# Performance work log

Hardware: AMD Instinct MI355X
Metric: run time of the kernel (lower is better)

Reference implementation:

```python
import jax, jax.numpy as jnp
import numpy as np

B, N, E1, H, D = 16, 256, 4, 8, 128  # batch, max nodes, edge types+1, heads, dim
VOCAB = 100


def setup_inputs() -> dict:
    key = jax.random.key(0)
    ks = jax.random.split(key, 20)
    s = 0.05
    return dict(
        node_feat=jax.random.randint(ks[0], (B, N), 0, VOCAB),
        L=jax.random.normal(ks[1], (B, N, N, E1), jnp.float32),
        emb=jax.random.normal(ks[2], (VOCAB, D), jnp.float32) * s,
        W0=jax.random.normal(ks[3], (E1, H, D, D), jnp.float32) * s,
        W1=jax.random.normal(ks[4], (E1, H, D * H * E1, D), jnp.float32) * (s / 4.0),
        a1w0=jax.random.normal(ks[5], (E1, H, D), jnp.float32) * s,
        a1b0=jnp.zeros((E1, H), jnp.float32),
        a2w0=jax.random.normal(ks[6], (E1, H, D), jnp.float32) * s,
        a2b0=jnp.zeros((E1, H), jnp.float32),
        a1w1=jax.random.normal(ks[7], (E1, H, D), jnp.float32) * s,
        a1b1=jnp.zeros((E1, H), jnp.float32),
        a2w1=jax.random.normal(ks[8], (E1, H, D), jnp.float32) * s,
        a2b1=jnp.zeros((E1, H), jnp.float32),
        sb0=jnp.zeros((E1, H, D), jnp.float32),
        sb1=jnp.zeros((E1, H, D), jnp.float32),
        outW=jax.random.normal(ks[9], (D, D), jnp.float32) * s,
        outb=jnp.zeros((D,), jnp.float32),
        attW=jax.random.normal(ks[10], (D,), jnp.float32) * s,
        attb=jnp.zeros((), jnp.float32),
    )


def _gat_layer(state, Ltr, W, a1w, a1b, a2w, a2b, sb, last):
    # state: (B, N, Din); W: (E1, H, Din, D); Ltr: (E1, 1, B, N, N)
    Wh = jnp.einsum('bni,ehio->ehbno', state, W)                      # (E1,H,B,N,D)
    s1 = jnp.einsum('ehbno,eho->ehbn', Wh, a1w) + a1b[:, :, None, None]
    s2 = jnp.einsum('ehbno,eho->ehbn', Wh, a2w) + a2b[:, :, None, None]
    logits = jax.nn.leaky_relu(s1[..., :, None] + s2[..., None, :], 0.2) + Ltr
    att = jax.nn.softmax(logits, axis=3)  # torch softmax over dim=1 of (B,N,N)
    h = jnp.einsum('ehbnm,ehbmo->ehbno', att, Wh) + sb[:, :, None, None, :]
    if last:
        return jnp.mean(h, axis=(0, 1))                               # (B,N,D)
    h = jax.nn.elu(h)
    # concat order in torch: outer edge-type jj, inner head ii -> (B,N,E1*H*D)
    return jnp.transpose(h, (2, 3, 0, 1, 4)).reshape(state.shape[0], state.shape[1], -1)


def reference(node_feat, L, emb, W0, W1, a1w0, a1b0, a2w0, a2b0,
              a1w1, a1b1, a2w1, a2b1, sb0, sb1, outW, outb, attW, attb):
    Ltr = jnp.transpose(L, (3, 0, 1, 2))[:, None]  # (E1,1,B,N,N)
    state = emb[node_feat]                         # (B,N,D)
    state = _gat_layer(state, Ltr, W0, a1w0, a1b0, a2w0, a2b0, sb0, last=False)
    state = _gat_layer(state, Ltr, W1, a1w1, a1b1, a2w1, a2b1, sb1, last=True)
    y = state @ outW + outb                        # (B,N,D)
    aw = jax.nn.sigmoid(state @ attW + attb)       # (B,N)
    y = aw[..., None] * y
    return jnp.mean(y, axis=1)                     # (B,D)
```

## Files before the change

### kernel.cpp

```cpp
#include <hip/hip_runtime.h>
#include <hip/hip_bf16.h>

#define Bq 16
#define Nq 256
#define E1q 4
#define Hq 8
#define Dq 128
#define EH 32
#define BN 4096

typedef __hip_bfloat16 bf16;
typedef short bf16x8 __attribute__((ext_vector_type(8)));
typedef float f32x4 __attribute__((ext_vector_type(4)));

__device__ __forceinline__ void gll16(const void* gptr, void* lptr) {
    __builtin_amdgcn_global_load_lds(
        (const __attribute__((address_space(1))) void*)gptr,
        (__attribute__((address_space(3))) void*)lptr, 16, 0, 0);
}

__device__ __forceinline__ unsigned short f2bf(float v) {
    __hip_bfloat16 h = __float2bfloat16(v);
    return *(unsigned short*)&h;
}

__device__ __forceinline__ void transpose_tile(const float* __restrict__ W,
                                               bf16* __restrict__ WT, int K,
                                               int kt, int nt, int eh,
                                               float (*tile)[65], int tid) {
    int tr = tid >> 6, tc = tid & 63;
    const float* src = W + ((size_t)eh * K + kt * 64) * 128 + nt * 64;
#pragma unroll
    for (int p = 0; p < 16; ++p) {
        int r = p * 4 + tr;
        tile[r][tc] = src[(size_t)r * 128 + tc];
    }
    __syncthreads();
    bf16* dst = WT + ((size_t)eh * 128 + nt * 64) * K + kt * 64;
#pragma unroll
    for (int p = 0; p < 16; ++p) {
        int n = p * 4 + tr;
        dst[(size_t)n * K + tc] = __float2bfloat16(tile[tc][n]);
    }
}

__global__ __launch_bounds__(256) void prep_kernel(const int* __restrict__ nf,
                                                   const float* __restrict__ emb,
                                                   const float* __restrict__ W0,
                                                   const float* __restrict__ W1,
                                                   const float* __restrict__ L,
                                                   bf16* __restrict__ st0b,
                                                   bf16* __restrict__ W0T,
                                                   bf16* __restrict__ W1T,
                                                   float* __restrict__ Le) {
    int bid = blockIdx.x;
    int t = threadIdx.x;
    __shared__ float tile[64][65];
    if (bid < 2048) {
        int i = bid * 256 + t;
        int row = i >> 7, col = i & 127;
        st0b[i] = __float2bfloat16(emb[nf[row] * Dq + col]);
    } else if (bid < 2176) {
        int id2 = bid - 2048;
        transpose_tile(W0, W0T, 128, id2 & 1, (id2 >> 1) & 1, id2 >> 2, tile, t);
    } else if (bid < 6272) {
        int id3 = bid - 2176;
        transpose_tile(W1, W1T, 4096, id3 & 63, (id3 >> 6) & 1, id3 >> 7, tile, t);
    } else {
        int idx = (bid - 6272) * 256 + t;
        float4 v = *(const float4*)(L + (size_t)idx * 4);
        Le[idx] = v.x;
        Le[1048576 + idx] = v.y;
        Le[2097152 + idx] = v.z;
        Le[3145728 + idx] = v.w;
    }
}

__global__ __launch_bounds__(256) void mfma_gemm_kernel(const bf16* __restrict__ Ab,
                                                        const bf16* __restrict__ Bt,
                                                        bf16* __restrict__ Wht,
                                                        const float* __restrict__ a1w,
                                                        const float* __restrict__ a1b,
                                                        const float* __restrict__ a2w,
                                                        const float* __restrict__ a2b,
                                                        float* __restrict__ s1,
                                                        float* __restrict__ s2, int K) {
    int id = blockIdx.x;
    int xcd = id & 7, slot = id >> 3;
    int eh = (slot & 3) * 8 + xcd;
    int rt = slot >> 2;
    int tid = threadIdx.x;
    int w = tid >> 6, l = tid & 63;
    int q = l >> 4, mn = l & 15;
    __shared__ __align__(16) bf16 As[128 * 64];
    __shared__ __align__(16) bf16 Bs[128 * 64];
    __shared__ float red1[128], red2[128];
    const bf16* Ap = Ab + (size_t)(rt * 128) * K;
    const bf16* Bp = Bt + (size_t)eh * 128 * K;
    int lr = l >> 3;
    int g = (l & 7) ^ lr;
    int gcol = g * 8;

    if (tid < 128) { red1[tid] = 0.f; red2[tid] = 0.f; }

    f32x4 acc[4][4];
#pragma unroll
    for (int i = 0; i < 4; i++)
#pragma unroll
        for (int j = 0; j < 4; j++) acc[i][j] = (f32x4){0.f, 0.f, 0.f, 0.f};

    int wr = (w >> 1) * 64, wc = (w & 1) * 64;
    int msw = mn & 7;

    for (int k0 = 0; k0 < K; k0 += 64) {
#pragma unroll
        for (int u = 0; u < 4; ++u) {
            int i = w * 4 + u;
            int r = i * 8 + lr;
            gll16(Ap + (size_t)r * K + k0 + gcol, (char*)As + i * 1024);
            gll16(Bp + (size_t)r * K + k0 + gcol, (char*)Bs + i * 1024);
        }
        __syncthreads();
#pragma unroll
        for (int kk = 0; kk < 2; ++kk) {
            int qb = ((kk * 4 + q) ^ msw) * 16;
            bf16x8 af[4], bfr[4];
#pragma unroll
            for (int i = 0; i < 4; ++i) {
                af[i]  = *(const bf16x8*)((const char*)As + (wr + i * 16 + mn) * 128 + qb);
                bfr[i] = *(const bf16x8*)((const char*)Bs + (wc + i * 16 + mn) * 128 + qb);
            }
#pragma unroll
            for (int i = 0; i < 4; ++i)
#pragma unroll
                for (int j = 0; j < 4; ++j)
                    acc[i][j] = __builtin_amdgcn_mfma_f32_16x16x32_bf16(af[i], bfr[j], acc[i][j], 0, 0, 0);
        }
        __syncthreads();
    }
#pragma unroll
    for (int i = 0; i < 4; ++i) {
        int r0 = rt * 128 + wr + i * 16 + q * 4;
        int b = r0 >> 8, m = r0 & 255;
#pragma unroll
        for (int j = 0; j < 4; ++j) {
            int o = wc + j * 16 + mn;
            ushort4 pk;
            pk.x = f2bf(acc[i][j][0]);
            pk.y = f2bf(acc[i][j][1]);
            pk.z = f2bf(acc[i][j][2]);
            pk.w = f2bf(acc[i][j][3]);
            *(ushort4*)(Wht + ((((size_t)eh * 16 + b) * 128 + o) * 256 + m)) = pk;
        }
    }
    float w1v[4], w2v[4];
#pragma unroll
    for (int j = 0; j < 4; ++j) {
        int o = wc + j * 16 + mn;
        w1v[j] = a1w[eh * 128 + o];
        w2v[j] = a2w[eh * 128 + o];
    }
#pragma unroll
    for (int i = 0; i < 4; ++i)
#pragma unroll
        for (int r = 0; r < 4; ++r) {
            float p1 = 0.f, p2 = 0.f;
#pragma unroll
            for (int j = 0; j < 4; ++j) {
                p1 += acc[i][j][r] * w1v[j];
                p2 += acc[i][j][r] * w2v[j];
            }
#pragma unroll
            for (int off = 1; off < 16; off <<= 1) {
                p1 += __shfl_xor(p1, off);
                p2 += __shfl_xor(p2, off);
            }
            if (mn == 0) {
                int row = wr + i * 16 + q * 4 + r;
                atomicAdd(&red1[row], p1);
                atomicAdd(&red2[row], p2);
            }
        }
    __syncthreads();
    if (tid < 128) {
        int rg = rt * 128 + tid;
        s1[eh * 4096 + rg] = red1[tid] + a1b[eh];
        s2[eh * 4096 + rg] = red2[tid] + a2b[eh];
    }
}

__global__ __launch_bounds__(512, 2) void gemm4k_kernel(const bf16* __restrict__ Ab,
                                                        const bf16* __restrict__ Bt,
                                                        bf16* __restrict__ Wht,
                                                        const float* __restrict__ a1w,
                                                        const float* __restrict__ a1b,
                                                        const float* __restrict__ a2w,
                                                        const float* __restrict__ a2b,
                                                        float* __restrict__ s1,
                                                        float* __restrict__ s2) {
    __shared__ __align__(16) char smem[131072];
    int bid = blockIdx.x;
    int wg = (bid & 7) * 32 + (bid >> 3);
    int tm = wg >> 4, tn = wg & 15;
    int tid = threadIdx.x;
    int wid = tid >> 6, l = tid & 63;
    int wr = wid >> 2, wc = wid & 3;
    int lhi = l >> 4, llo = l & 15;
    int skq = (l & 7) ^ ((l >> 3) & 7);

    const bf16* Ap = Ab + (size_t)tm * 256 * 4096;
    const bf16* Bp = Bt + (size_t)tn * 256 * 4096;
    const bf16* sA = Ap + (size_t)(wid * 8 + (l >> 3)) * 4096 + skq * 8;
    const bf16* sB = Bp + (size_t)(wid * 8 + (l >> 3)) * 4096 + skq * 8;
    char* dA = (char*)smem + wid * 1024;
    char* dB = (char*)smem + 32768 + wid * 1024;

    auto stA = [&](int tt, int s) {
        gll16(sA + (size_t)s * 64 * 4096 + tt * 64, dA + (tt & 1) * 65536 + s * 8192);
    };
    auto stB = [&](int tt, int s) {
        gll16(sB + (size_t)s * 64 * 4096 + tt * 64, dB + (tt & 1) * 65536 + s * 8192);
    };

    f32x4 acc[8][4];
#pragma unroll
    for (int i = 0; i < 8; ++i)
#pragma unroll
        for (int j = 0; j < 4; ++j) acc[i][j] = (f32x4){0.f, 0.f, 0.f, 0.f};

    int kp0 = ((lhi)     ^ (llo & 7)) << 4;
    int kp1 = ((4 + lhi) ^ (llo & 7)) << 4;
    int aoff = (wr * 64 + llo) << 7;
    int boff = 32768 + ((wc * 32 + llo) << 7);

    stA(0, 0); stA(0, 1); stB(0, 0); stB(0, 1);
    stA(0, 2); stA(0, 3); stB(0, 2); stB(0, 3);
    asm volatile("s_waitcnt vmcnt(4)" ::: "memory");
    __builtin_amdgcn_s_barrier();

#pragma unroll 1
    for (int t = 0; t < 64; ++t) {
        const char* sm = (const char*)smem + (t & 1) * 65536;
        bf16x8 A0[4][2], A1[4][2], B0[2][2], B1[2][2];
#pragma unroll
        for (int m = 0; m < 4; ++m) {
            A0[m][0] = *(const bf16x8*)(sm + aoff + m * 2048 + kp0);
            A0[m][1] = *(const bf16x8*)(sm + aoff + m * 2048 + kp1);
        }
#pragma unroll
        for (int n = 0; n < 2; ++n) {
            B0[n][0] = *(const bf16x8*)(sm + boff + n * 2048 + kp0);
            B0[n][1] = *(const bf16x8*)(sm + boff + n * 2048 + kp1);
        }
        if (t < 63) { stA(t + 1, 0); stA(t + 1, 1); }
        asm volatile("s_waitcnt lgkmcnt(8)" ::: "memory");
        __builtin_amdgcn_s_barrier();
        asm volatile("s_waitcnt lgkmcnt(0)" ::: "memory");
        __builtin_amdgcn_sched_barrier(0);
        __builtin_amdgcn_s_setprio(1);
#pragma unroll
        for (int ks = 0; ks < 2; ++ks)
#pragma unroll
            for (int m = 0; m < 4; ++m)
#pragma unroll
                for (int n = 0; n < 2; ++n)
                    acc[m][n] = __builtin_amdgcn_mfma_f32_16x16x32_bf16(A0[m][ks], B0[n][ks], acc[m][n], 0, 0, 0);
        __builtin_amdgcn_s_setprio(0);
        if (t < 63) { asm volatile("s_waitcnt vmcnt(4)" ::: "memory"); }
        else        { asm volatile("s_waitcnt vmcnt(2)" ::: "memory"); }
        __builtin_amdgcn_s_barrier();
#pragma unroll
        for (int m = 0; m < 4; ++m) {
            A1[m][0] = *(const bf16x8*)(sm + aoff + 16384 + m * 2048 + kp0);
            A1[m][1] = *(const bf16x8*)(sm + aoff + 16384 + m * 2048 + kp1);
        }
        if (t < 63) { stB(t + 1, 0); stB(t + 1, 1); }
        __builtin_amdgcn_s_barrier();
        asm volatile("s_waitcnt lgkmcnt(0)" ::: "memory");
        __builtin_amdgcn_sched_barrier(0);
        __builtin_amdgcn_s_setprio(1);
#pragma unroll
        for (int ks = 0; ks < 2; ++ks)
#pragma unroll
            for (int m = 0; m < 4; ++m)
#pragma unroll
                for (int n = 0; n < 2; ++n)
                    acc[4 + m][n] = __builtin_amdgcn_mfma_f32_16x16x32_bf16(A1[m][ks], B0[n][ks], acc[4 + m][n], 0, 0, 0);
        __builtin_amdgcn_s_setprio(0);
        if (t < 63) { asm volatile("s_waitcnt vmcnt(4)" ::: "memory"); }
        else        { asm volatile("s_waitcnt vmcnt(0)" ::: "memory"); }
        __builtin_amdgcn_s_barrier();
#pragma unroll
        for (int n = 0; n < 2; ++n) {
            B1[n][0] = *(const bf16x8*)(sm + boff + 16384 + n * 2048 + kp0);
            B1[n][1] = *(const bf16x8*)(sm + boff + 16384 + n * 2048 + kp1);
        }
        if (t < 63) { stA(t + 1, 2); stA(t + 1, 3); }
        __builtin_amdgcn_s_barrier();
        asm volatile("s_waitcnt lgkmcnt(0)" ::: "memory");
        __builtin_amdgcn_sched_barrier(0);
        __builtin_amdgcn_s_setprio(1);
#pragma unroll
        for (int ks = 0; ks < 2; ++ks)
#pragma unroll
            for (int m = 0; m < 4; ++m)
#pragma unroll
                for (int n = 0; n < 2; ++n)
                    acc[m][2 + n] = __builtin_amdgcn_mfma_f32_16x16x32_bf16(A0[m][ks], B1[n][ks], acc[m][2 + n], 0, 0, 0);
        __builtin_amdgcn_s_setprio(0);
        __builtin_amdgcn_s_barrier();
        if (t < 63) { stB(t + 1, 2); stB(t + 1, 3); }
        __builtin_amdgcn_s_setprio(1);
#pragma unroll
        for (int ks = 0; ks < 2; ++ks)
#pragma unroll
            for (int m = 0; m < 4; ++m)
#pragma unroll
                for (int n = 0; n < 2; ++n)
                    acc[4 + m][2 + n] = __builtin_amdgcn_mfma_f32_16x16x32_bf16(A1[m][ks], B1[n][ks], acc[4 + m][2 + n], 0, 0, 0);
        __builtin_amdgcn_s_setprio(0);
        if (t < 63) { asm volatile("s_waitcnt vmcnt(4)" ::: "memory"); }
        __builtin_amdgcn_s_barrier();
    }

    float* red = (float*)smem;
    red[tid] = 0.f;
    red[tid + 512] = 0.f;
    float w1v[4], w2v[4];
#pragma unroll
    for (int n = 0; n < 4; ++n) {
        int eh = tn * 2 + (n >> 1);
        int o = wc * 32 + (n & 1) * 16 + llo;
        w1v[n] = a1w[eh * 128 + o];
        w2v[n] = a2w[eh * 128 + o];
    }
    __syncthreads();
#pragma unroll
    for (int mi = 0; mi < 8; ++mi) {
        int R = (mi >> 2) * 128 + wr * 64 + (mi & 3) * 16 + lhi * 4;
#pragma unroll
        for (int n = 0; n < 4; ++n) {
            int eh = tn * 2 + (n >> 1);
            int o = wc * 32 + (n & 1) * 16 + llo;
            ushort4 pk;
            pk.x = f2bf(acc[mi][n][0]);
            pk.y = f2bf(acc[mi][n][1]);
            pk.z = f2bf(acc[mi][n][2]);
            pk.w = f2bf(acc[mi][n][3]);
            *(ushort4*)(Wht + ((((size_t)eh * 16 + tm) * 128 + o) * 256 + R)) = pk;
        }
#pragma unroll
        for (int r = 0; r < 4; ++r) {
            float p10 = acc[mi][0][r] * w1v[0] + acc[mi][1][r] * w1v[1];
            float p11 = acc[mi][2][r] * w1v[2] + acc[mi][3][r] * w1v[3];
            float p20 = acc[mi][0][r] * w2v[0] + acc[mi][1][r] * w2v[1];
            float p21 = acc[mi][2][r] * w2v[2] + acc[mi][3][r] * w2v[3];
#pragma unroll
            for (int off = 1; off < 16; off <<= 1) {
                p10 += __shfl_xor(p10, off);
                p11 += __shfl_xor(p11, off);
                p20 += __shfl_xor(p20, off);
                p21 += __shfl_xor(p21, off);
            }
            if (llo == 0) {
                int row = R + r;
                atomicAdd(&red[row], p10);
                atomicAdd(&red[256 + row], p11);
                atomicAdd(&red[512 + row], p20);
                atomicAdd(&red[768 + row], p21);
            }
        }
    }
    __syncthreads();
    {
        int ehl = tid >> 8, row = tid & 255;
        int eh = tn * 2 + ehl;
        s1[eh * 4096 + tm * 256 + row] = red[ehl * 256 + row] + a1b[eh];
        s2[eh * 4096 + tm * 256 + row] = red[512 + ehl * 256 + row] + a2b[eh];
    }
}

__global__ __launch_bounds__(256) void colsoft_kernel(const float* __restrict__ s1,
                                                      const float* __restrict__ s2,
                                                      const float* __restrict__ Le,
                                                      float4* __restrict__ stat) {
    int mt = blockIdx.x, b = blockIdx.y, e = blockIdx.z;
    int t = threadIdx.x;
    __shared__ float Lt[256 * 32];
    __shared__ float s1L[8 * 256];
#pragma unroll
    for (int i = 0; i < 8; ++i) s1L[i * 256 + t] = s1[(e * 8 + i) * 4096 + b * 256 + t];
    const float* Lb = Le + ((size_t)(e * 16 + b) * 256) * 256 + mt * 32;
#pragma unroll
    for (int j = 0; j < 8; ++j) {
        int f = t + 256 * j;
        int n = f >> 3, c4 = (f & 7) * 4;
        *(float4*)(Lt + n * 32 + c4) = *(const float4*)(Lb + (size_t)n * 256 + c4);
    }
    __syncthreads();
    int h = t >> 5, mm = t & 31;
    int m = mt * 32 + mm;
    float s2v = s2[(e * 8 + h) * 4096 + b * 256 + m];
    const float* s1p = s1L + h * 256;
    float s1max = -1e30f;
#pragma unroll
    for (int u = 0; u < 8; ++u) s1max = fmaxf(s1max, s1p[mm * 8 + u]);
#pragma unroll
    for (int off = 16; off; off >>= 1) s1max = fmaxf(s1max, __shfl_xor(s1max, off));
    float sm = s1max + s2v;
    float bound = (sm > 0.f ? sm : 0.2f * sm) + 8.0f;
    float sum = 0.f;
    for (int n = 0; n < 256; ++n) {
        float x = s1p[n] + s2v;
        x = x > 0.f ? x : 0.2f * x;
        x += Lt[n * 32 + mm];
        sum += __expf(x - bound);
    }
    float4 st = {s2v, bound, 1.0f / sum, 0.f};
    stat[(e * 8 + h) * 4096 + b * 256 + m] = st;
}

template <int LAST>
__global__ __launch_bounds__(256) void att_mfma_kernel(const float* __restrict__ s1,
                                                       const float4* __restrict__ stat,
                                                       const float* __restrict__ Le,
                                                       const bf16* __restrict__ Wht,
                                                       const float* __restrict__ sb,
                                                       bf16* __restrict__ outb) {
    int nt = blockIdx.x;
    int b = blockIdx.y;
    int eh = blockIdx.z;
    int e = eh >> 3;
    int tid = threadIdx.x;
    int w = tid >> 6, l = tid & 63;
    int q = l >> 4, mn = l & 15;
    __shared__ __align__(16) bf16 As[128 * 32];
    __shared__ __align__(16) bf16 Bs[128 * 40];
    __shared__ float s1L[128];
    __shared__ __align__(16) float4 stL[256];

    int base = eh * 4096 + b * 256;
    if (tid < 128) s1L[tid] = s1[base + nt * 128 + tid];
    stL[tid] = stat[base + tid];
    __syncthreads();

    const bf16* Whtp = Wht + ((size_t)eh * 16 + b) * 32768;
    int nl = tid >> 1, mh = (tid & 1) * 16;
    const float* Lrow = Le + (((size_t)(e * 16 + b) * 256) + nt * 128 + nl) * 256;
    float s1v = s1L[nl];
    int srow = l >> 2;
    int sq = (l & 3) ^ ((l >> 3) & 3);
    int scol = sq * 8;
    int rsw = ((mn >> 1) & 3) << 3;

    f32x4 acc[4][4];
#pragma unroll
    for (int i = 0; i < 4; i++)
#pragma unroll
        for (int j = 0; j < 4; j++) acc[i][j] = (f32x4){0.f, 0.f, 0.f, 0.f};

    int wr = (w >> 1) * 64, wc = (w & 1) * 64;

    float4 lv[4];
#pragma unroll
    for (int jj = 0; jj < 4; ++jj) lv[jj] = *(const float4*)(Lrow + mh + jj * 4);

    for (int k0 = 0; k0 < 256; k0 += 32) {
#pragma unroll
        for (int u = 0; u < 2; ++u) {
            int i = 2 * w + u;
            gll16(Whtp + (size_t)(i * 16 + srow) * 256 + k0 + scol, (char*)As + i * 1024);
        }
        float4 cur[4];
#pragma unroll
        for (int jj = 0; jj < 4; ++jj) cur[jj] = lv[jj];
        if (k0 + 32 < 256) {
#pragma unroll
            for (int jj = 0; jj < 4; ++jj)
                lv[jj] = *(const float4*)(Lrow + k0 + 32 + mh + jj * 4);
        }
#pragma unroll
        for (int jj = 0; jj < 4; ++jj) {
            int mb = mh + jj * 4;
            float av[4];
#pragma unroll
            for (int c = 0; c < 4; ++c) {
                int m = k0 + mb + c;
                float4 stv = stL[m];
                float x = s1v + stv.x;
                x = x > 0.f ? x : 0.2f * x;
                x += ((const float*)&cur[jj])[c];
                av[c] = __expf(x - stv.y) * stv.z;
            }
            unsigned int u01 = (unsigned int)f2bf(av[0]) | ((unsigned int)f2bf(av[1]) << 16);
            unsigned int u23 = (unsigned int)f2bf(av[2]) | ((unsigned int)f2bf(av[3]) << 16);
            unsigned int* bp = (unsigned int*)Bs + (nl * 40 + mb) / 2;
            bp[0] = u01;
            bp[1] = u23;
        }
        __syncthreads();
        bf16x8 af[4], bfr[4];
#pragma unroll
        for (int i = 0; i < 4; ++i) {
            af[i]  = *(const bf16x8*)(As + (wr + i * 16 + mn) * 32 + ((q << 3) ^ rsw));
            bfr[i] = *(const bf16x8*)(Bs + (wc + i * 16 + mn) * 40 + q * 8);
        }
#pragma unroll
        for (int i = 0; i < 4; ++i)
#pragma unroll
            for (int j = 0; j < 4; ++j)
                acc[i][j] = __builtin_amdgcn_mfma_f32_16x16x32_bf16(af[i], bfr[j], acc[i][j], 0, 0, 0);
        __syncthreads();
    }
#pragma unroll
    for (int i = 0; i < 4; ++i) {
        int o0 = wr + i * 16 + q * 4;
        float4 sbv = *(const float4*)(sb + eh * 128 + o0);
#pragma unroll
        for (int j = 0; j < 4; ++j) {
            int n = wc + j * 16 + mn;
            float v0 = acc[i][j][0] + sbv.x;
            float v1 = acc[i][j][1] + sbv.y;
            float v2 = acc[i][j][2] + sbv.z;
            float v3 = acc[i][j][3] + sbv.w;
            if (LAST == 0) {
                v0 = v0 > 0.f ? v0 : __expf(v0) - 1.f;
                v1 = v1 > 0.f ? v1 : __expf(v1) - 1.f;
                v2 = v2 > 0.f ? v2 : __expf(v2) - 1.f;
                v3 = v3 > 0.f ? v3 : __expf(v3) - 1.f;
                ushort4 pk = {f2bf(v0), f2bf(v1), f2bf(v2), f2bf(v3)};
                *(ushort4*)(outb + (size_t)(b * 256 + nt * 128 + n) * 4096 + eh * Dq + o0) = pk;
            } else {
                ushort4 pk = {f2bf(v0), f2bf(v1), f2bf(v2), f2bf(v3)};
                *(ushort4*)(outb + ((size_t)eh * 4096 + b * 256 + nt * 128 + n) * Dq + o0) = pk;
            }
        }
    }
}

__global__ __launch_bounds__(256) void reduce_aw_kernel(const bf16* __restrict__ h2b,
                                                        const float* __restrict__ attW,
                                                        const float* __restrict__ attb,
                                                        float* __restrict__ st2,
                                                        float* __restrict__ aw) {
    int t = threadIdx.x;
    int rl = t >> 7, o = t & 127;
    int r = blockIdx.x * 2 + rl;
    float acc = 0.f;
#pragma unroll
    for (int eh = 0; eh < EH; ++eh)
        acc += __bfloat162float(h2b[((size_t)eh * 4096 + r) * 128 + o]);
    acc *= (1.0f / 32.0f);
    st2[(size_t)r * 128 + o] = acc;
    float p = acc * attW[o];
#pragma unroll
    for (int off = 32; off; off >>= 1) p += __shfl_down(p, off);
    __shared__ float part[4];
    if ((t & 63) == 0) part[t >> 6] = p;
    __syncthreads();
    if (t == 0) aw[r] = 1.0f / (1.0f + __expf(-(part[0] + part[1] + attb[0])));
    if (t == 128) aw[r] = 1.0f / (1.0f + __expf(-(part[2] + part[3] + attb[0])));
}

__global__ __launch_bounds__(128) void final_kernel(const float* __restrict__ st2,
                                                    const float* __restrict__ aw,
                                                    const float* __restrict__ outW,
                                                    const float* __restrict__ outb,
                                                    float* __restrict__ out) {
    int b = blockIdx.x;
    int t = threadIdx.x;
    __shared__ float awL[256], zL[128];
    awL[t] = aw[b * 256 + t];
    awL[t + 128] = aw[b * 256 + t + 128];
    __syncthreads();
    float z = 0.f;
    for (int n = 0; n < 256; ++n) z += awL[n] * st2[(size_t)(b * 256 + n) * Dq + t];
    float sa = 0.f;
    for (int n = 0; n < 256; ++n) sa += awL[n];
    zL[t] = z;
    __syncthreads();
    float acc = sa * outb[t];
    for (int o = 0; o < Dq; ++o) acc += zL[o] * outW[o * Dq + t];
    out[b * Dq + t] = acc * (1.0f / 256.0f);
}

extern "C" void kernel_launch(void* const* d_in, const int* in_sizes, int n_in,
                              void* d_out, int out_size, void* d_ws, size_t ws_size,
                              hipStream_t stream) {
    const int* nf = (const int*)d_in[0];
    const float* L = (const float*)d_in[1];
    const float* emb = (const float*)d_in[2];
    const float* W0 = (const float*)d_in[3];
    const float* W1 = (const float*)d_in[4];
    const float* a1w0 = (const float*)d_in[5];
    const float* a1b0 = (const float*)d_in[6];
    const float* a2w0 = (const float*)d_in[7];
    const float* a2b0 = (const float*)d_in[8];
    const float* a1w1 = (const float*)d_in[9];
    const float* a1b1 = (const float*)d_in[10];
    const float* a2w1 = (const float*)d_in[11];
    const float* a2b1 = (const float*)d_in[12];
    const float* sb0 = (const float*)d_in[13];
    const float* sb1 = (const float*)d_in[14];
    const float* outW = (const float*)d_in[15];
    const float* outb = (const float*)d_in[16];
    const float* attW = (const float*)d_in[17];
    const float* attb = (const float*)d_in[18];

    char* p = (char*)d_ws;
    bf16* st0b = (bf16*)(p);
    bf16* W0T  = (bf16*)(p + 1048576);
    bf16* W1T  = (bf16*)(p + 2097152);
    bf16* st1b = (bf16*)(p + 35651584);
    bf16* h2b  = (bf16*)(p + 2097152);
    float* Le  = (float*)(p + 69206016);
    bf16* Wht  = (bf16*)(p + 85983232);
    float* s1  = (float*)(p + 119537664);
    float* s2  = (float*)(p + 120061952);
    float4* stat = (float4*)(p + 120586240);
    float* st2 = (float*)(p);
    float* aw  = s1;
    float* outp = (float*)d_out;

    prep_kernel<<<10368, 256, 0, stream>>>(nf, emb, W0, W1, L, st0b, W0T, W1T, Le);

    mfma_gemm_kernel<<<1024, 256, 0, stream>>>(st0b, W0T, Wht, a1w0, a1b0, a2w0, a2b0, s1, s2, 128);
    colsoft_kernel<<<dim3(8, 16, 4), 256, 0, stream>>>(s1, s2, Le, stat);
    att_mfma_kernel<0><<<dim3(2, 16, 32), 256, 0, stream>>>(s1, stat, Le, Wht, sb0, st1b);

    gemm4k_kernel<<<256, 512, 0, stream>>>(st1b, W1T, Wht, a1w1, a1b1, a2w1, a2b1, s1, s2);
    colsoft_kernel<<<dim3(8, 16, 4), 256, 0, stream>>>(s1, s2, Le, stat);
    att_mfma_kernel<1><<<dim3(2, 16, 32), 256, 0, stream>>>(s1, stat, Le, Wht, sb1, h2b);

    reduce_aw_kernel<<<2048, 256, 0, stream>>>(h2b, attW, attb, st2, aw);
    final_kernel<<<16, 128, 0, stream>>>(st2, aw, outW, outb, outp);
}
```

Baseline: 424.0 us.

## Software-pipeline LDS fragment loads one stage ahead of MFMA in GEMM main loop

```diff
diff --git a/kernel.cpp b/kernel.cpp
--- a/kernel.cpp
+++ b/kernel.cpp
@@ -237,24 +237,64 @@
     stA(0, 2); stA(0, 3); stB(0, 2); stB(0, 3);
     asm volatile("s_waitcnt vmcnt(4)" ::: "memory");
     __builtin_amdgcn_s_barrier();
+    bf16x8 A0[4][2], A1[4][2], B0[2][2], B1[2][2];
+    {
+        const char* sm0 = (const char*)smem;
+#pragma unroll
+        for (int m = 0; m < 4; ++m) {
+            A0[m][0] = *(const bf16x8*)(sm0 + aoff + m * 2048 + kp0);
+            A0[m][1] = *(const bf16x8*)(sm0 + aoff + m * 2048 + kp1);
+        }
+#pragma unroll
+        for (int n = 0; n < 2; ++n) {
+            B0[n][0] = *(const bf16x8*)(sm0 + boff + n * 2048 + kp0);
+            B0[n][1] = *(const bf16x8*)(sm0 + boff + n * 2048 + kp1);
+        }
+    }
+    asm volatile("s_waitcnt vmcnt(2)" ::: "memory");
+    __builtin_amdgcn_s_barrier();
 
 #pragma unroll 1
     for (int t = 0; t < 64; ++t) {
-        const char* sm = (const char*)smem + (t & 1) * 65536;
-        bf16x8 A0[4][2], A1[4][2], B0[2][2], B1[2][2];
+        const char* smc = (const char*)smem + (t & 1) * 65536;
+        const char* smn = (const char*)smem + (((t + 1) & 1)) * 65536;
 #pragma unroll
         for (int m = 0; m < 4; ++m) {
-            A0[m][0] = *(const bf16x8*)(sm + aoff + m * 2048 + kp0);
-            A0[m][1] = *(const bf16x8*)(sm + aoff + m * 2048 + kp1);
-        }
-#pragma unroll
-        for (int n = 0; n < 2; ++n) {
-            B0[n][0] = *(const bf16x8*)(sm + boff + n * 2048 + kp0);
-            B0[n][1] = *(const bf16x8*)(sm + boff + n * 2048 + kp1);
+            A1[m][0] = *(const bf16x8*)(smc + aoff + 16384 + m * 2048 + kp0);
+            A1[m][1] = *(const bf16x8*)(smc + aoff + 16384 + m * 2048 + kp1);
         }
         if (t < 63) { stA(t + 1, 0); stA(t + 1, 1); }
         asm volatile("s_waitcnt lgkmcnt(8)" ::: "memory");
+        __builtin_amdgcn_sched_barrier(0);
+        __builtin_amdgcn_s_setprio(1);
+#pragma unroll
+        for (int ks = 0; ks < 2; ++ks)
+#pragma unroll
+            for (int m = 0; m < 4; ++m)
+#pragma unroll
+                for (int n = 0; n < 2; ++n)
+                    acc[m][n] = __builtin_amdgcn_mfma_f32_16x16x32_bf16(A0[m][ks], B0[n][ks], acc[m][n], 0, 0, 0);
+        __builtin_amdgcn_s_setprio(0);
+        asm volatile("s_waitcnt vmcnt(2)" ::: "memory");
         __builtin_amdgcn_s_barrier();
+#pragma unroll
+        for (int n = 0; n < 2; ++n) {
+            B1[n][0] = *(const bf16x8*)(smc + boff + 16384 + n * 2048 + kp0);
+            B1[n][1] = *(const bf16x8*)(smc + boff + 16384 + n * 2048 + kp1);
+        }
+        if (t < 63) { stB(t + 1, 0); stB(t + 1, 1); }
+        asm volatile("s_waitcnt lgkmcnt(4)" ::: "memory");
+        __builtin_amdgcn_sched_barrier(0);
+        __builtin_amdgcn_s_setprio(1);
+#pragma unroll
+        for (int ks = 0; ks < 2; ++ks)
+#pragma unroll
+            for (int m = 0; m < 4; ++m)
+#pragma unroll
+                for (int n = 0; n < 2; ++n)
+                    acc[4 + m][n] = __builtin_amdgcn_mfma_f32_16x16x32_bf16(A1[m][ks], B0[n][ks], acc[4 + m][n], 0, 0, 0);
+        __builtin_amdgcn_s_setprio(0);
+        if (t < 63) { stA(t + 1, 2); stA(t + 1, 3); }
         asm volatile("s_waitcnt lgkmcnt(0)" ::: "memory");
         __builtin_amdgcn_sched_barrier(0);
         __builtin_amdgcn_s_setprio(1);
@@ -264,52 +304,24 @@
             for (int m = 0; m < 4; ++m)
 #pragma unroll
                 for (int n = 0; n < 2; ++n)
-                    acc[m][n] = __builtin_amdgcn_mfma_f32_16x16x32_bf16(A0[m][ks], B0[n][ks], acc[m][n], 0, 0, 0);
-        __builtin_amdgcn_s_setprio(0);
-        if (t < 63) { asm volatile("s_waitcnt vmcnt(4)" ::: "memory"); }
-        else        { asm volatile("s_waitcnt vmcnt(2)" ::: "memory"); }
-        __builtin_amdgcn_s_barrier();
-#pragma unroll
-        for (int m = 0; m < 4; ++m) {
-            A1[m][0] = *(const bf16x8*)(sm + aoff + 16384 + m * 2048 + kp0);
-            A1[m][1] = *(const bf16x8*)(sm + aoff + 16384 + m * 2048 + kp1);
-        }
-        if (t < 63) { stB(t + 1, 0); stB(t + 1, 1); }
-        __builtin_amdgcn_s_barrier();
-        asm volatile("s_waitcnt lgkmcnt(0)" ::: "memory");
-        __builtin_amdgcn_sched_barrier(0);
-        __builtin_amdgcn_s_setprio(1);
-#pragma unroll
-        for (int ks = 0; ks < 2; ++ks)
-#pragma unroll
-            for (int m = 0; m < 4; ++m)
-#pragma unroll
-                for (int n = 0; n < 2; ++n)
-                    acc[4 + m][n] = __builtin_amdgcn_mfma_f32_16x16x32_bf16(A1[m][ks], B0[n][ks], acc[4 + m][n], 0, 0, 0);
-        __builtin_amdgcn_s_setprio(0);
-        if (t < 63) { asm volatile("s_waitcnt vmcnt(4)" ::: "memory"); }
-        else        { asm volatile("s_waitcnt vmcnt(0)" ::: "memory"); }
-        __builtin_amdgcn_s_barrier();
-#pragma unroll
-        for (int n = 0; n < 2; ++n) {
-            B1[n][0] = *(const bf16x8*)(sm + boff + 16384 + n * 2048 + kp0);
-            B1[n][1] = *(const bf16x8*)(sm + boff + 16384 + n * 2048 + kp1);
-        }
-        if (t < 63) { stA(t + 1, 2); stA(t + 1, 3); }
-        __builtin_amdgcn_s_barrier();
-        asm volatile("s_waitcnt lgkmcnt(0)" ::: "memory");
-        __builtin_amdgcn_sched_barrier(0);
-        __builtin_amdgcn_s_setprio(1);
-#pragma unroll
-        for (int ks = 0; ks < 2; ++ks)
-#pragma unroll
-            for (int m = 0; m < 4; ++m)
-#pragma unroll
-                for (int n = 0; n < 2; ++n)
                     acc[m][2 + n] = __builtin_amdgcn_mfma_f32_16x16x32_bf16(A0[m][ks], B1[n][ks], acc[m][2 + n], 0, 0, 0);
         __builtin_amdgcn_s_setprio(0);
+        asm volatile("s_waitcnt vmcnt(2)" ::: "memory");
         __builtin_amdgcn_s_barrier();
-        if (t < 63) { stB(t + 1, 2); stB(t + 1, 3); }
+        if (t < 63) {
+#pragma unroll
+            for (int m = 0; m < 4; ++m) {
+                A0[m][0] = *(const bf16x8*)(smn + aoff + m * 2048 + kp0);
+                A0[m][1] = *(const bf16x8*)(smn + aoff + m * 2048 + kp1);
+            }
+#pragma unroll
+            for (int n = 0; n < 2; ++n) {
+                B0[n][0] = *(const bf16x8*)(smn + boff + n * 2048 + kp0);
+                B0[n][1] = *(const bf16x8*)(smn + boff + n * 2048 + kp1);
+            }
+            stB(t + 1, 2); stB(t + 1, 3);
+        }
+        __builtin_amdgcn_sched_barrier(0);
         __builtin_amdgcn_s_setprio(1);
 #pragma unroll
         for (int ks = 0; ks < 2; ++ks)
@@ -319,7 +331,7 @@
                 for (int n = 0; n < 2; ++n)
                     acc[4 + m][2 + n] = __builtin_amdgcn_mfma_f32_16x16x32_bf16(A1[m][ks], B1[n][ks], acc[4 + m][2 + n], 0, 0, 0);
         __builtin_amdgcn_s_setprio(0);
-        if (t < 63) { asm volatile("s_waitcnt vmcnt(4)" ::: "memory"); }
+        asm volatile("s_waitcnt vmcnt(2)" ::: "memory");
         __builtin_amdgcn_s_barrier();
     }
 
```

Result: faster. 411.6 us (-2.9%).
